# Kernel tuning notes

Measured on AMD Instinct MI355X. Metric: run time of the kernel, lower is better.

## Reference

```python
import jax, jax.numpy as jnp
import numpy as np

B, NB, PL, FD, H = 32, 64, 20, 4096, 1024


def setup_inputs() -> dict:
    key = jax.random.key(0)
    k1, k2, k3, k4, k5 = jax.random.split(key, 5)
    vision = jax.random.normal(k1, (B, NB, FD), dtype=jnp.float32)
    language = jax.random.normal(k2, (B, NB, PL, H), dtype=jnp.float32)
    phrase_lengths = jax.random.randint(k3, (B, NB), 1, PL + 1, dtype=jnp.int32)
    # Xavier-uniform initialized Linear params, zero bias (as in module)
    lim_v = float(np.sqrt(6.0 / (FD + H)))
    lim_l = float(np.sqrt(6.0 / (H + H)))
    Wv = jax.random.uniform(k4, (FD, H), minval=-lim_v, maxval=lim_v, dtype=jnp.float32)
    bv = jnp.zeros((H,), dtype=jnp.float32)
    Wl = jax.random.uniform(k5, (H, H), minval=-lim_l, maxval=lim_l, dtype=jnp.float32)
    bl = jnp.zeros((H,), dtype=jnp.float32)
    return {"vision": vision, "language": language, "phrase_lengths": phrase_lengths,
            "Wv": Wv, "bv": bv, "Wl": Wl, "bl": bl}


def reference(vision, language, phrase_lengths, Wv, bv, Wl, bl):
    # Vectorized replacement of the per-region loop: sum over phrase tokens,
    # divide by the (data-dependent) phrase length.  [B, NB, H]
    pooled = jnp.sum(language, axis=2) / phrase_lengths[..., None].astype(language.dtype)
    # Multimodal branch: both mappings applied.
    visual_map = jnp.einsum('bnf,fh->bnh', vision, Wv) + bv    # [B, NB, H]
    language_map = jnp.einsum('bnh,hk->bnk', pooled, Wl) + bl  # [B, NB, H]
    return (language_map, visual_map)
```

## Files before the change

kernel.cpp:

```cpp
#include <hip/hip_runtime.h>
#include <hip/hip_bf16.h>
#include <stdint.h>

#define B_   32
#define NB_  64
#define PL_  20
#define FD_  4096
#define H_   1024
#define M_   (B_ * NB_)

typedef short bf16x8 __attribute__((ext_vector_type(8)));
typedef float f32x4  __attribute__((ext_vector_type(4)));

__device__ __forceinline__ ushort f2bf(float f) {
    uint32_t u = __builtin_bit_cast(uint32_t, f);
    u += 0x7fffu + ((u >> 16) & 1u);
    return (ushort)(u >> 16);
}

__global__ __launch_bounds__(256) void prep_kernel(
    const float* __restrict__ lang, const int* __restrict__ plen,
    ushort* __restrict__ pooled,
    const float* __restrict__ vision, ushort* __restrict__ visionb,
    const float* __restrict__ Wv, ushort* __restrict__ WvT,
    const float* __restrict__ Wl, ushort* __restrict__ WlT,
    float* __restrict__ vis_zero)
{
    __shared__ float tile[32][33];
    int blk = blockIdx.x;
    int tid = threadIdx.x;

    if (blk < 2048) {
        int r = blk;
        int h = tid << 2;
        const float* base = lang + (size_t)r * (PL_ * H_) + h;
        float sx = 0.f, sy = 0.f, sz = 0.f, sw = 0.f;
#pragma unroll
        for (int p = 0; p < PL_; ++p) {
            float4 v = *(const float4*)(base + (size_t)p * H_);
            sx += v.x; sy += v.y; sz += v.z; sw += v.w;
        }
        float inv = 1.0f / (float)plen[r];
        ushort4 o = make_ushort4(f2bf(sx * inv), f2bf(sy * inv),
                                 f2bf(sz * inv), f2bf(sw * inv));
        *(ushort4*)(pooled + (size_t)r * H_ + h) = o;
    } else if (blk < 4096) {
        int base = (blk - 2048) * 1024 + tid;
#pragma unroll
        for (int it = 0; it < 4; ++it) {
            int i = base + it * 256;
            float4 v = ((const float4*)vision)[i];
            ushort4 o = make_ushort4(f2bf(v.x), f2bf(v.y), f2bf(v.z), f2bf(v.w));
            ((ushort4*)visionb)[i] = o;
        }
    } else if (blk < 6656) {
        const float* W; ushort* Wt; int K, b0;
        if (blk < 6144) { W = Wv; Wt = WvT; K = FD_; b0 = (blk - 4096) * 2; }
        else            { W = Wl; Wt = WlT; K = H_;  b0 = (blk - 6144) * 2; }
        int tx = tid & 31, ty = tid >> 5;
#pragma unroll
        for (int t = 0; t < 2; ++t) {
            int b = b0 + t;
            int n0 = (b & 31) * 32, k0 = (b >> 5) * 32;
#pragma unroll
            for (int i = 0; i < 32; i += 8)
                tile[ty + i][tx] = W[(size_t)(k0 + ty + i) * H_ + n0 + tx];
            __syncthreads();
#pragma unroll
            for (int i = 0; i < 32; i += 8)
                Wt[(size_t)(n0 + ty + i) * K + k0 + tx] = f2bf(tile[tx][ty + i]);
            __syncthreads();
        }
    } else {
        int base = (blk - 6656) * 1024 + tid;
#pragma unroll
        for (int it = 0; it < 4; ++it)
            ((float4*)vis_zero)[base + it * 256] =
                make_float4(0.f, 0.f, 0.f, 0.f);
    }
}

#define BM 128
#define BN 128
#define BK 64

__device__ __forceinline__ void async16(const void* g, void* l) {
    __builtin_amdgcn_global_load_lds(
        (const __attribute__((address_space(1))) void*)g,
        (__attribute__((address_space(3))) void*)l, 16, 0, 0);
}

__device__ __forceinline__ void stage_tile(
    const char* Ag, const char* Bg, size_t Kb, size_t ko,
    char* AsB, char* BsB, int tid)
{
#pragma unroll
    for (int j = 0; j < 4; ++j) {
        int off = j * 4096 + tid * 16;
        int row = off >> 7;
        int cbl = off & 127;
        int cbg = cbl ^ ((row & 7) << 4);
        async16(Ag + (size_t)row * Kb + ko + cbg, AsB + off);
        async16(Bg + (size_t)row * Kb + ko + cbg, BsB + off);
    }
}

__global__ __launch_bounds__(256) void gemm_bt_dual(
    const ushort* __restrict__ A1, const ushort* __restrict__ Bt1,
    const float* __restrict__ bias1, float* __restrict__ C1,
    const ushort* __restrict__ A2, const ushort* __restrict__ Bt2,
    const float* __restrict__ bias2, float* __restrict__ C2)
{
    __shared__ ushort As[2][BM * BK];
    __shared__ ushort Bs[2][BN * BK];

    int wg = blockIdx.x;
    bool isV = wg < 384;
    int w, ks, nk, k0s;
    if (isV) {
        ks = wg >> 7;
        w  = wg & 127;
        nk  = (ks == 0) ? 22 : 21;
        k0s = (ks == 0) ? 0 : (22 + (ks - 1) * 21);
    } else {
        ks = 0; w = wg - 384; nk = 16; k0s = 0;
    }
    int y = w & 7, x = w >> 3;

    const ushort* A   = isV ? A1 : A2;
    const ushort* Bt  = isV ? Bt1 : Bt2;
    const float* bias = isV ? bias1 : bias2;
    float* C          = isV ? C1 : C2;
    int K             = isV ? FD_ : H_;

    const int N = H_;
    int tid  = threadIdx.x;
    int wave = tid >> 6, lane = tid & 63;
    int lx = lane & 15, lz = lane >> 4;
    int wr = wave >> 1, wc = wave & 1;
    int row0 = x * BM;
    int col0 = y * BN;

    size_t Kb = (size_t)K * 2;

    const char* Ag = (const char*)A  + (size_t)row0 * Kb;
    const char* Bg = (const char*)Bt + (size_t)col0 * Kb;

    int sw = (lx & 7) << 4;

    f32x4 acc[4][4] = {};

    stage_tile(Ag, Bg, Kb, (size_t)k0s * 128,       (char*)As[0], (char*)Bs[0], tid);
    stage_tile(Ag, Bg, Kb, (size_t)(k0s + 1) * 128, (char*)As[1], (char*)Bs[1], tid);

    for (int kt = 0; kt < nk; ++kt) {
        if (kt < nk - 1) asm volatile("s_waitcnt vmcnt(8)" ::: "memory");
        else             asm volatile("s_waitcnt vmcnt(0)" ::: "memory");
        __builtin_amdgcn_s_barrier();

        const char* Ab = (const char*)As[kt & 1];
        const char* Bb = (const char*)Bs[kt & 1];
        bf16x8 af[2][4], bfr[2][4];
#pragma unroll
        for (int kk = 0; kk < 2; ++kk) {
#pragma unroll
            for (int m = 0; m < 4; ++m)
                af[kk][m] = *(const bf16x8*)(Ab +
                    (wr * 64 + m * 16 + lx) * 128 + ((kk * 64 + lz * 16) ^ sw));
#pragma unroll
            for (int n = 0; n < 4; ++n)
                bfr[kk][n] = *(const bf16x8*)(Bb +
                    (wc * 64 + n * 16 + lx) * 128 + ((kk * 64 + lz * 16) ^ sw));
        }
#pragma unroll
        for (int kk = 0; kk < 2; ++kk)
#pragma unroll
            for (int m = 0; m < 4; ++m)
#pragma unroll
                for (int n = 0; n < 4; ++n)
                    acc[m][n] = __builtin_amdgcn_mfma_f32_16x16x32_bf16(
                        af[kk][m], bfr[kk][n], acc[m][n], 0, 0, 0);

        __builtin_amdgcn_s_barrier();
        if (kt + 2 < nk)
            stage_tile(Ag, Bg, Kb, (size_t)(k0s + kt + 2) * 128,
                       (char*)As[kt & 1], (char*)Bs[kt & 1], tid);
    }

#pragma unroll
    for (int m = 0; m < 4; ++m) {
        int row = row0 + wr * 64 + m * 16 + lz * 4;
#pragma unroll
        for (int n = 0; n < 4; ++n) {
            int col = col0 + wc * 64 + n * 16 + lx;
            float bb = (ks == 0) ? bias[col] : 0.f;
            if (isV) {
#pragma unroll
                for (int r = 0; r < 4; ++r)
                    atomicAdd(&C[(size_t)(row + r) * N + col],
                              acc[m][n][r] + bb);
            } else {
#pragma unroll
                for (int r = 0; r < 4; ++r)
                    C[(size_t)(row + r) * N + col] = acc[m][n][r] + bb;
            }
        }
    }
}

extern "C" void kernel_launch(void* const* d_in, const int* in_sizes, int n_in,
                              void* d_out, int out_size, void* d_ws, size_t ws_size,
                              hipStream_t stream) {
    const float* vision   = (const float*)d_in[0];
    const float* language = (const float*)d_in[1];
    const int*   plen     = (const int*)d_in[2];
    const float* Wv       = (const float*)d_in[3];
    const float* bv       = (const float*)d_in[4];
    const float* Wl       = (const float*)d_in[5];
    const float* bl       = (const float*)d_in[6];

    float* out      = (float*)d_out;
    float* lang_map = out;
    float* vis_map  = out + (size_t)M_ * H_;

    char* ws = (char*)d_ws;
    ushort* pooled  = (ushort*)(ws);
    ushort* visionb = (ushort*)(ws + (4u  << 20));
    ushort* WvT     = (ushort*)(ws + (20u << 20));
    ushort* WlT     = (ushort*)(ws + (28u << 20));

    hipLaunchKernelGGL(prep_kernel, dim3(7168), dim3(256), 0, stream,
                       language, plen, pooled, vision, visionb,
                       Wv, WvT, Wl, WlT, vis_map);
    hipLaunchKernelGGL(gemm_bt_dual, dim3(512), dim3(256), 0, stream,
                       visionb, WvT, bv, vis_map,
                       pooled,  WlT, bl, lang_map);
}
```

Before: 87.27 us.

## Enlarge GEMM tiles to 256x256 with 512 threads and split-K both GEMMs

Doubles the GEMM block tile to 256x256 with 8 waves per block. The vision GEMM becomes a 6-way split-K and the language GEMM a 2-way split-K, so 256 blocks fill roughly one per CU. Both outputs are now zeroed in the prep kernel and accumulated with atomics. The aim is more operand reuse per LDS load and better load balance. In exchange there is less latency hiding (128KB LDS per block allows only one block per CU, despite the launch bound asking for two) and extra atomic traffic on the language output.

```diff
diff --git a/kernel.cpp b/kernel.cpp
--- a/kernel.cpp
+++ b/kernel.cpp
@@ -24,7 +24,7 @@
     const float* __restrict__ vision, ushort* __restrict__ visionb,
     const float* __restrict__ Wv, ushort* __restrict__ WvT,
     const float* __restrict__ Wl, ushort* __restrict__ WlT,
-    float* __restrict__ vis_zero)
+    float* __restrict__ out_zero)
 {
     __shared__ float tile[32][33];
     int blk = blockIdx.x;
@@ -75,13 +75,13 @@
         int base = (blk - 6656) * 1024 + tid;
 #pragma unroll
         for (int it = 0; it < 4; ++it)
-            ((float4*)vis_zero)[base + it * 256] =
+            ((float4*)out_zero)[base + it * 256] =
                 make_float4(0.f, 0.f, 0.f, 0.f);
     }
 }
 
-#define BM 128
-#define BN 128
+#define BM 256
+#define BN 256
 #define BK 64
 
 __device__ __forceinline__ void async16(const void* g, void* l) {
@@ -96,7 +96,7 @@
 {
 #pragma unroll
     for (int j = 0; j < 4; ++j) {
-        int off = j * 4096 + tid * 16;
+        int off = j * 8192 + tid * 16;
         int row = off >> 7;
         int cbl = off & 127;
         int cbg = cbl ^ ((row & 7) << 4);
@@ -105,7 +105,7 @@
     }
 }
 
-__global__ __launch_bounds__(256) void gemm_bt_dual(
+__global__ __launch_bounds__(512, 2) void gemm_bt_dual(
     const ushort* __restrict__ A1, const ushort* __restrict__ Bt1,
     const float* __restrict__ bias1, float* __restrict__ C1,
     const ushort* __restrict__ A2, const ushort* __restrict__ Bt2,
@@ -115,17 +115,20 @@
     __shared__ ushort Bs[2][BN * BK];
 
     int wg = blockIdx.x;
-    bool isV = wg < 384;
+    bool isV = wg < 192;
     int w, ks, nk, k0s;
     if (isV) {
-        ks = wg >> 7;
-        w  = wg & 127;
-        nk  = (ks == 0) ? 22 : 21;
-        k0s = (ks == 0) ? 0 : (22 + (ks - 1) * 21);
+        ks = wg >> 5;
+        w  = wg & 31;
+        nk  = (ks < 4) ? 11 : 10;
+        k0s = (ks < 4) ? ks * 11 : 44 + (ks - 4) * 10;
     } else {
-        ks = 0; w = wg - 384; nk = 16; k0s = 0;
-    }
-    int y = w & 7, x = w >> 3;
+        int v = wg - 192;
+        ks = v >> 5;
+        w  = v & 31;
+        nk = 8; k0s = ks * 8;
+    }
+    int y = w & 3, x = w >> 2;
 
     const ushort* A   = isV ? A1 : A2;
     const ushort* Bt  = isV ? Bt1 : Bt2;
@@ -137,7 +140,7 @@
     int tid  = threadIdx.x;
     int wave = tid >> 6, lane = tid & 63;
     int lx = lane & 15, lz = lane >> 4;
-    int wr = wave >> 1, wc = wave & 1;
+    int wr = wave >> 2, wc = wave & 3;
     int row0 = x * BM;
     int col0 = y * BN;
 
@@ -148,7 +151,7 @@
 
     int sw = (lx & 7) << 4;
 
-    f32x4 acc[4][4] = {};
+    f32x4 acc[8][4] = {};
 
     stage_tile(Ag, Bg, Kb, (size_t)k0s * 128,       (char*)As[0], (char*)Bs[0], tid);
     stage_tile(Ag, Bg, Kb, (size_t)(k0s + 1) * 128, (char*)As[1], (char*)Bs[1], tid);
@@ -160,26 +163,24 @@
 
         const char* Ab = (const char*)As[kt & 1];
         const char* Bb = (const char*)Bs[kt & 1];
-        bf16x8 af[2][4], bfr[2][4];
 #pragma unroll
         for (int kk = 0; kk < 2; ++kk) {
-#pragma unroll
-            for (int m = 0; m < 4; ++m)
-                af[kk][m] = *(const bf16x8*)(Ab +
-                    (wr * 64 + m * 16 + lx) * 128 + ((kk * 64 + lz * 16) ^ sw));
+            bf16x8 af[8], bfr[4];
+#pragma unroll
+            for (int m = 0; m < 8; ++m)
+                af[m] = *(const bf16x8*)(Ab +
+                    (wr * 128 + m * 16 + lx) * 128 + ((kk * 64 + lz * 16) ^ sw));
 #pragma unroll
             for (int n = 0; n < 4; ++n)
-                bfr[kk][n] = *(const bf16x8*)(Bb +
+                bfr[n] = *(const bf16x8*)(Bb +
                     (wc * 64 + n * 16 + lx) * 128 + ((kk * 64 + lz * 16) ^ sw));
-        }
-#pragma unroll
-        for (int kk = 0; kk < 2; ++kk)
-#pragma unroll
-            for (int m = 0; m < 4; ++m)
+#pragma unroll
+            for (int m = 0; m < 8; ++m)
 #pragma unroll
                 for (int n = 0; n < 4; ++n)
                     acc[m][n] = __builtin_amdgcn_mfma_f32_16x16x32_bf16(
-                        af[kk][m], bfr[kk][n], acc[m][n], 0, 0, 0);
+                        af[m], bfr[n], acc[m][n], 0, 0, 0);
+        }
 
         __builtin_amdgcn_s_barrier();
         if (kt + 2 < nk)
@@ -188,22 +189,16 @@
     }
 
 #pragma unroll
-    for (int m = 0; m < 4; ++m) {
-        int row = row0 + wr * 64 + m * 16 + lz * 4;
+    for (int m = 0; m < 8; ++m) {
+        int row = row0 + wr * 128 + m * 16 + lz * 4;
 #pragma unroll
         for (int n = 0; n < 4; ++n) {
             int col = col0 + wc * 64 + n * 16 + lx;
             float bb = (ks == 0) ? bias[col] : 0.f;
-            if (isV) {
-#pragma unroll
-                for (int r = 0; r < 4; ++r)
-                    atomicAdd(&C[(size_t)(row + r) * N + col],
-                              acc[m][n][r] + bb);
-            } else {
-#pragma unroll
-                for (int r = 0; r < 4; ++r)
-                    C[(size_t)(row + r) * N + col] = acc[m][n][r] + bb;
-            }
+#pragma unroll
+            for (int r = 0; r < 4; ++r)
+                atomicAdd(&C[(size_t)(row + r) * N + col],
+                          acc[m][n][r] + bb);
         }
     }
 }
@@ -229,10 +224,10 @@
     ushort* WvT     = (ushort*)(ws + (20u << 20));
     ushort* WlT     = (ushort*)(ws + (28u << 20));
 
-    hipLaunchKernelGGL(prep_kernel, dim3(7168), dim3(256), 0, stream,
+    hipLaunchKernelGGL(prep_kernel, dim3(7680), dim3(256), 0, stream,
                        language, plen, pooled, vision, visionb,
-                       Wv, WvT, Wl, WlT, vis_map);
-    hipLaunchKernelGGL(gemm_bt_dual, dim3(512), dim3(256), 0, stream,
+                       Wv, WvT, Wl, WlT, out);
+    hipLaunchKernelGGL(gemm_bt_dual, dim3(256), dim3(512), 0, stream,
                        visionb, WvT, bv, vis_map,
                        pooled,  WlT, bl, lang_map);
 }
```

Result: slower. 112.2 us (+28.5%).
